# Performance work log

Measured on AMD Instinct MI355X. Metric: run time of the kernel, lower is better.

## Reference

```python
import jax, jax.numpy as jnp
import numpy as np

B, SEQ_LEN, PRED_LEN, LABEL_LEN, PERIOD, N_CH = 32, 2048, 1024, 512, 256, 256
K = SEQ_LEN // PERIOD   # seg_num_x = 8
L = PRED_LEN // PERIOD  # seg_num_y = 4
EPS = 1e-5


def setup_inputs() -> dict:
    key = jax.random.key(0)
    k1, k2, k3, k4, k5, k6, k7 = jax.random.split(key, 7)
    x_enc = jax.random.normal(k1, (B, SEQ_LEN, N_CH), jnp.float32)
    x_mark_enc = jax.random.normal(k2, (B, SEQ_LEN, 4), jnp.float32)
    x_dec = jax.random.normal(k3, (B, LABEL_LEN + PRED_LEN, N_CH), jnp.float32)
    x_mark_dec = jax.random.normal(k4, (B, LABEL_LEN + PRED_LEN, 4), jnp.float32)
    # base_model abstracted as a linear map on the time axis of a [B, PERIOD, N] segment.
    # Scaled ~1/sqrt(P) so repeated powers (up to K+L-1 = 11) stay numerically tame.
    W_base = jax.random.normal(k5, (PERIOD, PERIOD), jnp.float32) * (0.9 / np.sqrt(PERIOD))
    # new_encoders[j]: nn.Linear(seg_num_x, 1) -> weight row [K] + bias scalar per j.
    W_enc = jax.random.normal(k6, (L, K), jnp.float32) * (1.0 / np.sqrt(K))
    b_enc = jax.random.normal(k7, (L,), jnp.float32) * 0.01
    return {"x_enc": x_enc, "x_mark_enc": x_mark_enc, "x_dec": x_dec,
            "x_mark_dec": x_mark_dec, "W_base": W_base, "W_enc": W_enc, "b_enc": b_enc}


def reference(x_enc, x_mark_enc, x_dec, x_mark_dec, W_base, W_enc, b_enc):
    Bv, S, N = x_enc.shape
    # per-series normalization over time (means is .detach()'d in torch; fwd math identical)
    means = jnp.mean(x_enc, axis=1, keepdims=True)                  # [B,1,N]
    xc = x_enc - means
    stdev = jnp.sqrt(jnp.var(xc, axis=1, keepdims=True) + EPS)      # [B,1,N]
    xn = xc / stdev

    # split into K segments of length PERIOD: [K, B, P, N]
    segs = xn.reshape(Bv, K, PERIOD, N).transpose(1, 0, 2, 3)

    # x_res[l][k] = base_model applied (K - k + l) times to segment k.
    # base(x) = einsum('qp,bpn->bqn', W_base, x), so m applications = W_base^m.
    def step(c, _):
        nxt = W_base @ c
        return nxt, nxt
    _, rest = jax.lax.scan(step, W_base, None, length=K + L - 2)
    powers = jnp.concatenate([W_base[None], rest], axis=0)          # powers[i] = W^(i+1)

    exps = (K - jnp.arange(K))[None, :] + jnp.arange(L)[:, None]    # [L,K]
    Wlk = powers[exps - 1]                                          # [L,K,P,P]
    x_res = jnp.einsum('lkqp,kbpn->lkbqn', Wlk, segs)               # [L,K,B,P,N]

    # dec_out_part[l] = sum_k W_enc[l,k] * x_res[l][k] + b_enc[l] * ones
    dec = jnp.einsum('lk,lkbqn->lbqn', W_enc, x_res) + b_enc[:, None, None, None]
    dec = dec.transpose(1, 0, 2, 3).reshape(Bv, L * PERIOD, N)      # cat over time

    # de-normalize
    dec = dec * stdev[:, 0, :][:, None, :] + means[:, 0, :][:, None, :]
    return dec[:, -PRED_LEN:, :]
```

## Files before the change

kernel.cpp:

```cpp
#include <hip/hip_runtime.h>
#include <cstdint>
#include <cstddef>


typedef unsigned short ushort_t;
typedef unsigned int uint_t;
typedef __attribute__((ext_vector_type(8))) short bf16x8;
typedef __attribute__((ext_vector_type(16))) float f32x16;

__device__ __forceinline__ ushort_t f32_to_bf16(float f) {
    uint_t u = __float_as_uint(f);
    u += 0x7FFFu + ((u >> 16) & 1u);
    return (ushort_t)(u >> 16);
}
__device__ __forceinline__ float bf16_to_f32(ushort_t h) {
    return __uint_as_float((uint_t)h << 16);
}

struct PowOps { int sa[4]; int sb[4]; int sd[4]; int ed[4]; };

__global__ void powmulc(const float* __restrict__ Wb, float* __restrict__ Pw,
                        ushort_t* __restrict__ Pb, float* __restrict__ prs, PowOps ops) {
    __shared__ float As[4 * 256];
    __shared__ float red[4][4];
    const int mat = blockIdx.x;
    const int r0  = blockIdx.y * 4;
    const int tid = threadIdx.x;
    const int e   = ops.ed[mat];
    const int sa  = ops.sa[mat];
    float a[4];
    if (sa == -2) {
#pragma unroll
        for (int i = 0; i < 4; ++i) a[i] = (r0 + i == tid) ? 1.0f : 0.0f;
    } else if (sa == -3) {
#pragma unroll
        for (int i = 0; i < 4; ++i) a[i] = Wb[(size_t)(r0 + i) * 256 + tid];
    } else {
        const float* A  = (sa < 0) ? Wb : Pw + (size_t)sa * 65536;
        const float* Bm = (ops.sb[mat] < 0) ? Wb : Pw + (size_t)ops.sb[mat] * 65536;
#pragma unroll
        for (int i = 0; i < 4; ++i) As[i * 256 + tid] = A[(size_t)(r0 + i) * 256 + tid];
        __syncthreads();
        float a0 = 0.f, a1 = 0.f, a2 = 0.f, a3 = 0.f;
        for (int p = 0; p < 256; p += 8) {
            float bv[8];
#pragma unroll
            for (int u = 0; u < 8; ++u) bv[u] = Bm[(size_t)(p + u) * 256 + tid];
#pragma unroll
            for (int u = 0; u < 8; ++u) {
                a0 += As[0 * 256 + p + u] * bv[u];
                a1 += As[1 * 256 + p + u] * bv[u];
                a2 += As[2 * 256 + p + u] * bv[u];
                a3 += As[3 * 256 + p + u] * bv[u];
            }
        }
        a[0] = a0; a[1] = a1; a[2] = a2; a[3] = a3;
        if (ops.sd[mat] >= 0) {
            float* C = Pw + (size_t)ops.sd[mat] * 65536;
#pragma unroll
            for (int i = 0; i < 4; ++i) C[(size_t)(r0 + i) * 256 + tid] = a[i];
        }
        __syncthreads();
    }
    const int lane = tid & 63, wv = tid >> 6;
    float rs[4];
#pragma unroll
    for (int i = 0; i < 4; ++i) {
        const ushort_t h = f32_to_bf16(a[i]);
        Pb[(size_t)e * 65536 + (size_t)(r0 + i) * 256 + tid] = h;
        float v = bf16_to_f32(h);
        v += __shfl_xor(v, 1);  v += __shfl_xor(v, 2);  v += __shfl_xor(v, 4);
        v += __shfl_xor(v, 8);  v += __shfl_xor(v, 16); v += __shfl_xor(v, 32);
        rs[i] = v;
    }
    if (lane == 0) {
#pragma unroll
        for (int i = 0; i < 4; ++i) red[i][wv] = rs[i];
    }
    __syncthreads();
    if (tid < 4) prs[e * 256 + r0 + tid] = red[tid][0] + red[tid][1] + red[tid][2] + red[tid][3];
}

__global__ void prep(const float* __restrict__ x, ushort_t* __restrict__ Xt,
                     float* __restrict__ ps1, float* __restrict__ ps2) {
    __shared__ float lds[64 * 65];
    __shared__ float red1[16 * 64];
    __shared__ float red2[16 * 64];
    const int bid = blockIdx.x;
    const int st = bid & 31;
    const int nt = (bid >> 5) & 3;
    const int b  = bid >> 7;
    const int tid = threadIdx.x;
    const int c = tid & 15, r = tid >> 4;
    const int s0 = st * 64;
    float s1[4] = {0,0,0,0}, s2[4] = {0,0,0,0};
#pragma unroll
    for (int it = 0; it < 4; ++it) {
        const int ii = r + it * 16;
        const float4 v = *(const float4*)(x + ((size_t)b * 2048 + s0 + ii) * 256 + nt * 64 + c * 4);
        const float vv[4] = {v.x, v.y, v.z, v.w};
#pragma unroll
        for (int jj = 0; jj < 4; ++jj) {
            lds[ii * 65 + c * 4 + jj] = vv[jj];
            s1[jj] += vv[jj]; s2[jj] += vv[jj] * vv[jj];
        }
    }
#pragma unroll
    for (int jj = 0; jj < 4; ++jj) { red1[r * 64 + c * 4 + jj] = s1[jj]; red2[r * 64 + c * 4 + jj] = s2[jj]; }
    __syncthreads();
    if (tid < 64) {
        float a = 0.f, q = 0.f;
#pragma unroll
        for (int rr = 0; rr < 16; ++rr) { a += red1[rr * 64 + tid]; q += red2[rr * 64 + tid]; }
        const size_t o = (size_t)st * 8192 + b * 256 + nt * 64 + tid;
        ps1[o] = a; ps2[o] = q;
    }
#pragma unroll
    for (int step = 0; step < 8; ++step) {
        const int npr = step * 8 + (tid >> 5);
        const int sp  = (tid & 31) * 2;
        const float f0 = lds[sp * 65 + npr];
        const float f1 = lds[(sp + 1) * 65 + npr];
        const uint_t packed = (uint_t)f32_to_bf16(f0) | ((uint_t)f32_to_bf16(f1) << 16);
        *(uint_t*)(Xt + ((size_t)b * 256 + nt * 64 + npr) * 2048 + s0 + sp) = packed;
    }
}

#define GLOAD_LDS16(gsrc, ldst) \
    __builtin_amdgcn_global_load_lds((const __attribute__((address_space(1))) void*)(gsrc), \
                                     (__attribute__((address_space(3))) void*)(ldst), 16, 0, 0)

__global__ __launch_bounds__(256, 2) void gemm_v(
    const ushort_t* __restrict__ Pb,
    const ushort_t* __restrict__ Xt,
    ushort_t* __restrict__ vt)
{
    __shared__ ushort_t sAa[3][4096];
    __shared__ ushort_t sBb[3][8192];

    const int bid = blockIdx.x;
    const int tid = threadIdx.x;

    const int xcd  = bid & 7;
    const int g    = bid >> 3;
    const int colT = xcd + ((g & 7) << 3);
    const int k    = g >> 3;
    const int e    = 8 - k;

    const int lane = tid & 63;
    const int w    = tid >> 6;
    const int wm   = w >> 1, wn = w & 1;
    const int li   = lane & 31, lg = lane >> 5;
    const int lq3  = (li >> 1) & 3;
    const int lrow = 2 * (lane >> 3) + ((lane >> 2) & 1);
    const int kc   = (lane & 3) ^ ((lane >> 3) & 3);

    const ushort_t* xtb = Xt + (size_t)(colT * 128) * 2048 + k * 256;
    const ushort_t* pbb = Pb + (size_t)e * 65536;

#define VSTAGE(bf_, kt_) do { \
    const int p0_ = (kt_) * 32 + kc * 8; \
    GLOAD_LDS16(xtb + (size_t)(w * 32 + 0  + lrow) * 2048 + p0_, &sAa[bf_][(w * 32 + 0)  * 32]); \
    GLOAD_LDS16(xtb + (size_t)(w * 32 + 16 + lrow) * 2048 + p0_, &sAa[bf_][(w * 32 + 16) * 32]); \
    GLOAD_LDS16(pbb + (w * 64 + 0  + lrow) * 256 + p0_, &sBb[bf_][(w * 64 + 0)  * 32]); \
    GLOAD_LDS16(pbb + (w * 64 + 16 + lrow) * 256 + p0_, &sBb[bf_][(w * 64 + 16) * 32]); \
    GLOAD_LDS16(pbb + (w * 64 + 32 + lrow) * 256 + p0_, &sBb[bf_][(w * 64 + 32) * 32]); \
    GLOAD_LDS16(pbb + (w * 64 + 48 + lrow) * 256 + p0_, &sBb[bf_][(w * 64 + 48) * 32]); \
} while (0)

    f32x16 acc[2][4];
#pragma unroll
    for (int mm = 0; mm < 2; ++mm)
#pragma unroll
        for (int nn = 0; nn < 4; ++nn)
#pragma unroll
            for (int rr = 0; rr < 16; ++rr) acc[mm][nn][rr] = 0.0f;

    VSTAGE(0, 0);
    VSTAGE(1, 1);

#define VKT(kt_) do { \
    if ((kt_) < 7) { asm volatile("s_waitcnt vmcnt(6)" ::: "memory"); } \
    else           { asm volatile("s_waitcnt vmcnt(0)" ::: "memory"); } \
    __builtin_amdgcn_s_barrier(); \
    asm volatile("" ::: "memory"); \
    const ushort_t* pa_ = &sAa[(kt_) % 3][0]; \
    const ushort_t* px_ = &sBb[(kt_) % 3][0]; \
    bf16x8 af[2][2], xf[2][4]; \
    _Pragma("unroll") \
    for (int ks = 0; ks < 2; ++ks) { \
        const int sl = ((ks << 1) + lg) ^ lq3; \
        const int ro = (li >> 1) * 64 + (li & 1) * 32 + sl * 8; \
        af[ks][0] = *(const bf16x8*)(pa_ + wm * 2048 + ro); \
        af[ks][1] = *(const bf16x8*)(pa_ + wm * 2048 + 1024 + ro); \
        xf[ks][0] = *(const bf16x8*)(px_ + wn * 4096 + ro); \
        xf[ks][1] = *(const bf16x8*)(px_ + wn * 4096 + 1024 + ro); \
        xf[ks][2] = *(const bf16x8*)(px_ + wn * 4096 + 2048 + ro); \
        xf[ks][3] = *(const bf16x8*)(px_ + wn * 4096 + 3072 + ro); \
    } \
    if ((kt_) < 6) { VSTAGE(((kt_) + 2) % 3, (kt_) + 2); } \
    __builtin_amdgcn_s_setprio(1); \
    _Pragma("unroll") \
    for (int ks = 0; ks < 2; ++ks) \
        _Pragma("unroll") \
        for (int mm = 0; mm < 2; ++mm) \
            _Pragma("unroll") \
            for (int nn = 0; nn < 4; ++nn) \
                acc[mm][nn] = __builtin_amdgcn_mfma_f32_32x32x16_bf16(af[ks][mm], xf[ks][nn], acc[mm][nn], 0, 0, 0); \
    __builtin_amdgcn_s_setprio(0); \
    asm volatile("" ::: "memory"); \
} while (0)

    VKT(0); VKT(1); VKT(2); VKT(3); VKT(4); VKT(5); VKT(6); VKT(7);
#undef VKT
#undef VSTAGE

    ushort_t* vb = vt + (size_t)k * 2097152;
#pragma unroll
    for (int mm = 0; mm < 2; ++mm)
#pragma unroll
        for (int nn = 0; nn < 4; ++nn) {
            const int q = wn * 128 + nn * 32 + li;
#pragma unroll
            for (int rr = 0; rr < 16; ++rr) {
                const int c = colT * 128 + wm * 64 + mm * 32 + ((rr & 3) + 8 * (rr >> 2) + 4 * lg);
                vb[(size_t)c * 256 + q] = f32_to_bf16(acc[mm][nn][rr]);
            }
        }
}

__global__ void combine(const ushort_t* __restrict__ vt, const float* __restrict__ Wenc,
                        ushort_t* __restrict__ c,
                        const float* __restrict__ ps1, const float* __restrict__ ps2,
                        const float* __restrict__ prs, const ushort_t* __restrict__ Pb,
                        float* __restrict__ meanv, float* __restrict__ stdv,
                        float* __restrict__ rsA) {
    __shared__ float uf[256];
    const int bid = blockIdx.x;
    const int t   = threadIdx.x;
    if (bid < 1024) {
        const int col = bid * 8 + (t >> 5);
        const size_t off = (size_t)col * 256 + (t & 31) * 8;
        float a0[8] = {0,0,0,0,0,0,0,0}, a1[8] = {0,0,0,0,0,0,0,0};
        float a2[8] = {0,0,0,0,0,0,0,0}, a3[8] = {0,0,0,0,0,0,0,0};
#pragma unroll
        for (int k = 0; k < 8; ++k) {
            const bf16x8 v = *(const bf16x8*)(vt + (size_t)k * 2097152 + off);
            const float w0 = Wenc[0 * 8 + k], w1 = Wenc[1 * 8 + k];
            const float w2 = Wenc[2 * 8 + k], w3 = Wenc[3 * 8 + k];
#pragma unroll
            for (int j = 0; j < 8; ++j) {
                const float f = bf16_to_f32((ushort_t)v[j]);
                a0[j] += w0 * f; a1[j] += w1 * f; a2[j] += w2 * f; a3[j] += w3 * f;
            }
        }
        bf16x8 o0, o1, o2, o3;
#pragma unroll
        for (int j = 0; j < 8; ++j) {
            o0[j] = (short)f32_to_bf16(a0[j]); o1[j] = (short)f32_to_bf16(a1[j]);
            o2[j] = (short)f32_to_bf16(a2[j]); o3[j] = (short)f32_to_bf16(a3[j]);
        }
        *(bf16x8*)(c + 0 * 2097152 + off) = o0;
        *(bf16x8*)(c + 1 * 2097152 + off) = o1;
        *(bf16x8*)(c + 2 * 2097152 + off) = o2;
        *(bf16x8*)(c + 3 * 2097152 + off) = o3;
    } else if (bid < 1056) {
        const int b = bid - 1024;
        float s = 0.f, q = 0.f;
#pragma unroll
        for (int st = 0; st < 32; ++st) {
            s += ps1[(size_t)st * 8192 + b * 256 + t];
            q += ps2[(size_t)st * 8192 + b * 256 + t];
        }
        const float mean = s * (1.0f / 2048.0f);
        float var = q * (1.0f / 2048.0f) - mean * mean;
        var = fmaxf(var, 0.0f);
        meanv[b * 256 + t] = mean;
        stdv [b * 256 + t] = sqrtf(var + 1e-5f);
    } else {
        const int l = bid - 1056;
        float u = 0.f;
#pragma unroll
        for (int k = 0; k < 8; ++k) u += Wenc[l * 8 + k] * prs[(8 - k) * 256 + t];
        uf[t] = u;
        __syncthreads();
        const uint2* rp = (const uint2*)(Pb + (size_t)l * 65536 + t * 256);
        float s = 0.f;
#pragma unroll
        for (int i = 0; i < 64; ++i) {
            const uint2 v = rp[i];
            s += bf16_to_f32((ushort_t)(v.x & 0xffff)) * uf[i * 4 + 0]
               + bf16_to_f32((ushort_t)(v.x >> 16))    * uf[i * 4 + 1]
               + bf16_to_f32((ushort_t)(v.y & 0xffff)) * uf[i * 4 + 2]
               + bf16_to_f32((ushort_t)(v.y >> 16))    * uf[i * 4 + 3];
        }
        rsA[l * 256 + t] = s;
    }
}

__global__ __launch_bounds__(256, 2) void gemm2(
    const ushort_t* __restrict__ Pb, const ushort_t* __restrict__ c,
    const float* __restrict__ meanv, const float* __restrict__ stdv,
    const float* __restrict__ rsA, const float* __restrict__ benc,
    float* __restrict__ out)
{
    __shared__ ushort_t sAa[3][4096];
    __shared__ ushort_t sBb[3][4096];

    const int bid  = blockIdx.x;
    const int xcd  = bid & 7;
    const int g    = bid >> 3;
    const int colT = xcd + ((g & 7) << 3);
    const int rest = g >> 3;
    const int l    = rest >> 1;
    const int qpT  = rest & 1;

    const int tid  = threadIdx.x;
    const int lane = tid & 63;
    const int w    = tid >> 6;
    const int wm   = w >> 1, wn = w & 1;
    const int li   = lane & 31, lg = lane >> 5;
    const int lq3  = (li >> 1) & 3;
    const int lrow = 2 * (lane >> 3) + ((lane >> 2) & 1);
    const int kc   = (lane & 3) ^ ((lane >> 3) & 3);

    const ushort_t* ab = Pb + (size_t)l * 65536 + (size_t)(qpT * 128) * 256;
    const ushort_t* cb = c + ((size_t)l * 8192 + colT * 128) * 256;

#define GSTAGE(bf_, kt_) do { \
    const int p0_ = (kt_) * 32 + kc * 8; \
    GLOAD_LDS16(ab + (w * 32 + 0  + lrow) * 256 + p0_, &sAa[bf_][(w * 32 + 0)  * 32]); \
    GLOAD_LDS16(ab + (w * 32 + 16 + lrow) * 256 + p0_, &sAa[bf_][(w * 32 + 16) * 32]); \
    GLOAD_LDS16(cb + (w * 32 + 0  + lrow) * 256 + p0_, &sBb[bf_][(w * 32 + 0)  * 32]); \
    GLOAD_LDS16(cb + (w * 32 + 16 + lrow) * 256 + p0_, &sBb[bf_][(w * 32 + 16) * 32]); \
} while (0)

    f32x16 acc[2][2];
#pragma unroll
    for (int mm = 0; mm < 2; ++mm)
#pragma unroll
        for (int nn = 0; nn < 2; ++nn)
#pragma unroll
            for (int rr = 0; rr < 16; ++rr) acc[mm][nn][rr] = 0.0f;

    GSTAGE(0, 0);
    GSTAGE(1, 1);

#define GKT(kt_) do { \
    if ((kt_) < 7) { asm volatile("s_waitcnt vmcnt(4)" ::: "memory"); } \
    else           { asm volatile("s_waitcnt vmcnt(0)" ::: "memory"); } \
    __builtin_amdgcn_s_barrier(); \
    asm volatile("" ::: "memory"); \
    const ushort_t* pa_ = &sAa[(kt_) % 3][0]; \
    const ushort_t* px_ = &sBb[(kt_) % 3][0]; \
    bf16x8 af[2][2], xf[2][2]; \
    _Pragma("unroll") \
    for (int ks = 0; ks < 2; ++ks) { \
        const int sl = ((ks << 1) + lg) ^ lq3; \
        const int ro = (li >> 1) * 64 + (li & 1) * 32 + sl * 8; \
        af[ks][0] = *(const bf16x8*)(pa_ + wm * 2048 + ro); \
        af[ks][1] = *(const bf16x8*)(pa_ + wm * 2048 + 1024 + ro); \
        xf[ks][0] = *(const bf16x8*)(px_ + wn * 2048 + ro); \
        xf[ks][1] = *(const bf16x8*)(px_ + wn * 2048 + 1024 + ro); \
    } \
    if ((kt_) < 6) { GSTAGE(((kt_) + 2) % 3, (kt_) + 2); } \
    __builtin_amdgcn_s_setprio(1); \
    _Pragma("unroll") \
    for (int ks = 0; ks < 2; ++ks) { \
        acc[0][0] = __builtin_amdgcn_mfma_f32_32x32x16_bf16(af[ks][0], xf[ks][0], acc[0][0], 0, 0, 0); \
        acc[0][1] = __builtin_amdgcn_mfma_f32_32x32x16_bf16(af[ks][0], xf[ks][1], acc[0][1], 0, 0, 0); \
        acc[1][0] = __builtin_amdgcn_mfma_f32_32x32x16_bf16(af[ks][1], xf[ks][0], acc[1][0], 0, 0, 0); \
        acc[1][1] = __builtin_amdgcn_mfma_f32_32x32x16_bf16(af[ks][1], xf[ks][1], acc[1][1], 0, 0, 0); \
    } \
    __builtin_amdgcn_s_setprio(0); \
    asm volatile("" ::: "memory"); \
} while (0)

    GKT(0); GKT(1); GKT(2); GKT(3); GKT(4); GKT(5); GKT(6); GKT(7);
#undef GKT
#undef GSTAGE

    const float be = benc[l];
    float mn[2], sd[2];
#pragma unroll
    for (int nn = 0; nn < 2; ++nn) {
        const int col = colT * 128 + wn * 64 + nn * 32 + li;
        mn[nn] = meanv[col];
        sd[nn] = stdv [col];
    }
#pragma unroll
    for (int mm = 0; mm < 2; ++mm)
#pragma unroll
        for (int nn = 0; nn < 2; ++nn) {
            const int col = colT * 128 + wn * 64 + nn * 32 + li;
            const int bq = col >> 8, nq = col & 255;
            const float ben = be * sd[nn];
#pragma unroll
            for (int rr = 0; rr < 16; ++rr) {
                const int trow = l * 256 + qpT * 128 + wm * 64 + mm * 32
                               + ((rr & 3) + 8 * (rr >> 2) + 4 * lg);
                out[((size_t)bq * 1024 + trow) * 256 + nq] =
                    acc[mm][nn][rr] + mn[nn] * (1.0f - rsA[trow]) + ben;
            }
        }
}

extern "C" void kernel_launch(void* const* d_in, const int* in_sizes, int n_in,
                              void* d_out, int out_size, void* d_ws, size_t ws_size,
                              hipStream_t stream) {
    (void)in_sizes; (void)n_in; (void)out_size; (void)ws_size;
    const float* x_enc  = (const float*)d_in[0];
    const float* W_base = (const float*)d_in[4];
    const float* W_enc  = (const float*)d_in[5];
    const float* b_enc  = (const float*)d_in[6];
    float* out = (float*)d_out;

    char* ws = (char*)d_ws;
    float*    wsP    = (float*)(ws);
    ushort_t* wsPb   = (ushort_t*)(ws + 0x200000);
    float*    wsPrs  = (float*)(ws + 0x340000);
    float*    wsS1   = (float*)(ws + 0x350000);
    float*    wsS2   = (float*)(ws + 0x450000);
    float*    wsMean = (float*)(ws + 0x550000);
    float*    wsStd  = (float*)(ws + 0x560000);
    float*    wsRsA  = (float*)(ws + 0x570000);
    ushort_t* wsXt   = (ushort_t*)(ws + 0x600000);
    ushort_t* wsC    = (ushort_t*)(ws + 0x600000);
    ushort_t* wsVt   = (ushort_t*)(ws + 0x2600000);

    { PowOps o{{-1, -3, -2, 0}, {-1, 0, 0, 0}, {0, -1, -1, 0}, {2, 1, 0, 0}};
      powmulc<<<dim3(3, 64), 256, 0, stream>>>(W_base, wsP, wsPb, wsPrs, o); }
    { PowOps o{{0, 0, 0, 0}, {-1, 0, 0, 0}, {1, 2, 0, 0}, {3, 4, 0, 0}};
      powmulc<<<dim3(2, 64), 256, 0, stream>>>(W_base, wsP, wsPb, wsPrs, o); }
    { PowOps o{{2, 2, 2, 2}, {-1, 0, 1, 2}, {-1, -1, -1, -1}, {5, 6, 7, 8}};
      powmulc<<<dim3(4, 64), 256, 0, stream>>>(W_base, wsP, wsPb, wsPrs, o); }

    prep<<<4096, 256, 0, stream>>>(x_enc, wsXt, wsS1, wsS2);

    gemm_v<<<512, 256, 0, stream>>>(wsPb, wsXt, wsVt);

    combine<<<1060, 256, 0, stream>>>(wsVt, W_enc, wsC, wsS1, wsS2, wsPrs, wsPb,
                                      wsMean, wsStd, wsRsA);

    gemm2<<<512, 256, 0, stream>>>(wsPb, wsC, wsMean, wsStd, wsRsA, b_enc, out);
}
```

Before: 99.64 us.

## Fuse combine into second GEMM and fold stats/rowsum into gemm_v

Removes the separate combine kernel. The W_enc-weighted reduction over the eight vt slices now runs inside a new 512-thread gemm2c kernel, which writes the combined bf16 tile straight to LDS and feeds it to MFMA, so the intermediate c buffer never goes through global memory. The mean/std and rsA side computations move into extra blocks appended to the gemm_v launch. This saves one launch and a full write-plus-read of c, but each gemm2c block reads all eight vt slices per k-tile, and it changes the block count, LDS footprint and occupancy.

```diff
diff --git a/kernel.cpp b/kernel.cpp
--- a/kernel.cpp
+++ b/kernel.cpp
@@ -133,13 +133,53 @@
 __global__ __launch_bounds__(256, 2) void gemm_v(
     const ushort_t* __restrict__ Pb,
     const ushort_t* __restrict__ Xt,
-    ushort_t* __restrict__ vt)
+    ushort_t* __restrict__ vt,
+    const float* __restrict__ ps1, const float* __restrict__ ps2,
+    const float* __restrict__ prs, const float* __restrict__ Wenc,
+    float* __restrict__ meanv, float* __restrict__ stdv, float* __restrict__ rsA)
 {
     __shared__ ushort_t sAa[3][4096];
     __shared__ ushort_t sBb[3][8192];
 
     const int bid = blockIdx.x;
     const int tid = threadIdx.x;
+    if (bid >= 512) {
+        const int idx = bid - 512;
+        if (idx < 32) {
+            const int b = idx;
+            float s = 0.f, q = 0.f;
+#pragma unroll
+            for (int st = 0; st < 32; ++st) {
+                s += ps1[(size_t)st * 8192 + b * 256 + tid];
+                q += ps2[(size_t)st * 8192 + b * 256 + tid];
+            }
+            const float mean = s * (1.0f / 2048.0f);
+            float var = q * (1.0f / 2048.0f) - mean * mean;
+            var = fmaxf(var, 0.0f);
+            meanv[b * 256 + tid] = mean;
+            stdv [b * 256 + tid] = sqrtf(var + 1e-5f);
+        } else {
+            const int l = idx - 32;
+            float u = 0.f;
+#pragma unroll
+            for (int k = 0; k < 8; ++k) u += Wenc[l * 8 + k] * prs[(8 - k) * 256 + tid];
+            float* uf = (float*)&sAa[0][0];
+            uf[tid] = u;
+            __syncthreads();
+            const uint2* rp = (const uint2*)(Pb + (size_t)l * 65536 + tid * 256);
+            float s = 0.f;
+#pragma unroll
+            for (int i = 0; i < 64; ++i) {
+                const uint2 v = rp[i];
+                s += bf16_to_f32((ushort_t)(v.x & 0xffff)) * uf[i * 4 + 0]
+                   + bf16_to_f32((ushort_t)(v.x >> 16))    * uf[i * 4 + 1]
+                   + bf16_to_f32((ushort_t)(v.y & 0xffff)) * uf[i * 4 + 2]
+                   + bf16_to_f32((ushort_t)(v.y >> 16))    * uf[i * 4 + 3];
+            }
+            rsA[l * 256 + tid] = s;
+        }
+        return;
+    }
 
     const int xcd  = bid & 7;
     const int g    = bid >> 3;
@@ -229,110 +269,80 @@
         }
 }
 
-__global__ void combine(const ushort_t* __restrict__ vt, const float* __restrict__ Wenc,
-                        ushort_t* __restrict__ c,
-                        const float* __restrict__ ps1, const float* __restrict__ ps2,
-                        const float* __restrict__ prs, const ushort_t* __restrict__ Pb,
-                        float* __restrict__ meanv, float* __restrict__ stdv,
-                        float* __restrict__ rsA) {
-    __shared__ float uf[256];
-    const int bid = blockIdx.x;
-    const int t   = threadIdx.x;
-    if (bid < 1024) {
-        const int col = bid * 8 + (t >> 5);
-        const size_t off = (size_t)col * 256 + (t & 31) * 8;
-        float a0[8] = {0,0,0,0,0,0,0,0}, a1[8] = {0,0,0,0,0,0,0,0};
-        float a2[8] = {0,0,0,0,0,0,0,0}, a3[8] = {0,0,0,0,0,0,0,0};
-#pragma unroll
-        for (int k = 0; k < 8; ++k) {
-            const bf16x8 v = *(const bf16x8*)(vt + (size_t)k * 2097152 + off);
-            const float w0 = Wenc[0 * 8 + k], w1 = Wenc[1 * 8 + k];
-            const float w2 = Wenc[2 * 8 + k], w3 = Wenc[3 * 8 + k];
-#pragma unroll
-            for (int j = 0; j < 8; ++j) {
-                const float f = bf16_to_f32((ushort_t)v[j]);
-                a0[j] += w0 * f; a1[j] += w1 * f; a2[j] += w2 * f; a3[j] += w3 * f;
-            }
-        }
-        bf16x8 o0, o1, o2, o3;
-#pragma unroll
-        for (int j = 0; j < 8; ++j) {
-            o0[j] = (short)f32_to_bf16(a0[j]); o1[j] = (short)f32_to_bf16(a1[j]);
-            o2[j] = (short)f32_to_bf16(a2[j]); o3[j] = (short)f32_to_bf16(a3[j]);
-        }
-        *(bf16x8*)(c + 0 * 2097152 + off) = o0;
-        *(bf16x8*)(c + 1 * 2097152 + off) = o1;
-        *(bf16x8*)(c + 2 * 2097152 + off) = o2;
-        *(bf16x8*)(c + 3 * 2097152 + off) = o3;
-    } else if (bid < 1056) {
-        const int b = bid - 1024;
-        float s = 0.f, q = 0.f;
-#pragma unroll
-        for (int st = 0; st < 32; ++st) {
-            s += ps1[(size_t)st * 8192 + b * 256 + t];
-            q += ps2[(size_t)st * 8192 + b * 256 + t];
-        }
-        const float mean = s * (1.0f / 2048.0f);
-        float var = q * (1.0f / 2048.0f) - mean * mean;
-        var = fmaxf(var, 0.0f);
-        meanv[b * 256 + t] = mean;
-        stdv [b * 256 + t] = sqrtf(var + 1e-5f);
-    } else {
-        const int l = bid - 1056;
-        float u = 0.f;
-#pragma unroll
-        for (int k = 0; k < 8; ++k) u += Wenc[l * 8 + k] * prs[(8 - k) * 256 + t];
-        uf[t] = u;
-        __syncthreads();
-        const uint2* rp = (const uint2*)(Pb + (size_t)l * 65536 + t * 256);
-        float s = 0.f;
-#pragma unroll
-        for (int i = 0; i < 64; ++i) {
-            const uint2 v = rp[i];
-            s += bf16_to_f32((ushort_t)(v.x & 0xffff)) * uf[i * 4 + 0]
-               + bf16_to_f32((ushort_t)(v.x >> 16))    * uf[i * 4 + 1]
-               + bf16_to_f32((ushort_t)(v.y & 0xffff)) * uf[i * 4 + 2]
-               + bf16_to_f32((ushort_t)(v.y >> 16))    * uf[i * 4 + 3];
-        }
-        rsA[l * 256 + t] = s;
-    }
-}
-
-__global__ __launch_bounds__(256, 2) void gemm2(
-    const ushort_t* __restrict__ Pb, const ushort_t* __restrict__ c,
+__global__ __launch_bounds__(512, 2) void gemm2c(
+    const ushort_t* __restrict__ Pb, const ushort_t* __restrict__ vt,
+    const float* __restrict__ Wenc,
     const float* __restrict__ meanv, const float* __restrict__ stdv,
     const float* __restrict__ rsA, const float* __restrict__ benc,
     float* __restrict__ out)
 {
-    __shared__ ushort_t sAa[3][4096];
-    __shared__ ushort_t sBb[3][4096];
+    __shared__ ushort_t sAa[3][16384];
+    __shared__ ushort_t sCc[2][8192];
 
     const int bid  = blockIdx.x;
     const int xcd  = bid & 7;
     const int g    = bid >> 3;
-    const int colT = xcd + ((g & 7) << 3);
-    const int rest = g >> 3;
-    const int l    = rest >> 1;
-    const int qpT  = rest & 1;
+    const int colH = xcd + ((g & 15) << 3);
+    const int qc   = g >> 4;
 
     const int tid  = threadIdx.x;
     const int lane = tid & 63;
     const int w    = tid >> 6;
-    const int wm   = w >> 1, wn = w & 1;
+    const int l    = w & 3;
+    const int qh   = w >> 2;
     const int li   = lane & 31, lg = lane >> 5;
     const int lq3  = (li >> 1) & 3;
     const int lrow = 2 * (lane >> 3) + ((lane >> 2) & 1);
     const int kc   = (lane & 3) ^ ((lane >> 3) & 3);
 
-    const ushort_t* ab = Pb + (size_t)l * 65536 + (size_t)(qpT * 128) * 256;
-    const ushort_t* cb = c + ((size_t)l * 8192 + colT * 128) * 256;
-
-#define GSTAGE(bf_, kt_) do { \
+    const int ccol = tid & 63;
+    const int qoct = (tid >> 6) & 3;
+    const int rep  = tid >> 8;
+
+    const ushort_t* ab = Pb + (size_t)l * 65536 + (size_t)(qc * 128) * 256;
+    const ushort_t* vb = vt + (size_t)(colH * 64 + ccol) * 256;
+
+    float weR[2][8];
+#pragma unroll
+    for (int j = 0; j < 2; ++j)
+#pragma unroll
+        for (int k = 0; k < 8; ++k) weR[j][k] = Wenc[(rep * 2 + j) * 8 + k];
+    asm volatile("s_waitcnt vmcnt(0)" ::: "memory");
+
+#define AST(bf_, kt_) do { \
     const int p0_ = (kt_) * 32 + kc * 8; \
-    GLOAD_LDS16(ab + (w * 32 + 0  + lrow) * 256 + p0_, &sAa[bf_][(w * 32 + 0)  * 32]); \
-    GLOAD_LDS16(ab + (w * 32 + 16 + lrow) * 256 + p0_, &sAa[bf_][(w * 32 + 16) * 32]); \
-    GLOAD_LDS16(cb + (w * 32 + 0  + lrow) * 256 + p0_, &sBb[bf_][(w * 32 + 0)  * 32]); \
-    GLOAD_LDS16(cb + (w * 32 + 16 + lrow) * 256 + p0_, &sBb[bf_][(w * 32 + 16) * 32]); \
+    _Pragma("unroll") \
+    for (int i_ = 0; i_ < 4; ++i_) \
+        GLOAD_LDS16(ab + (size_t)(qh * 64 + i_ * 16 + lrow) * 256 + p0_, \
+                    &sAa[bf_][l * 4096 + qh * 2048 + i_ * 512]); \
+} while (0)
+
+#define VLOAD(dst_, kt_) do { \
+    _Pragma("unroll") \
+    for (int k_ = 0; k_ < 8; ++k_) \
+        dst_[k_] = *(const bf16x8*)(vb + (size_t)k_ * 2097152 + (kt_) * 32 + qoct * 8); \
+} while (0)
+
+#define COMB(src_, cb_) do { \
+    _Pragma("unroll") \
+    for (int j_ = 0; j_ < 2; ++j_) { \
+        float s_[8] = {0,0,0,0,0,0,0,0}; \
+        _Pragma("unroll") \
+        for (int k_ = 0; k_ < 8; ++k_) { \
+            const float w_ = weR[j_][k_]; \
+            _Pragma("unroll") \
+            for (int q_ = 0; q_ < 8; ++q_) \
+                s_[q_] += w_ * bf16_to_f32((ushort_t)src_[k_][q_]); \
+        } \
+        uint4 o_; \
+        o_.x = (uint_t)f32_to_bf16(s_[0]) | ((uint_t)f32_to_bf16(s_[1]) << 16); \
+        o_.y = (uint_t)f32_to_bf16(s_[2]) | ((uint_t)f32_to_bf16(s_[3]) << 16); \
+        o_.z = (uint_t)f32_to_bf16(s_[4]) | ((uint_t)f32_to_bf16(s_[5]) << 16); \
+        o_.w = (uint_t)f32_to_bf16(s_[6]) | ((uint_t)f32_to_bf16(s_[7]) << 16); \
+        const int le_ = (rep * 2 + j_) * 2048 + (ccol >> 1) * 64 + (ccol & 1) * 32 \
+                      + ((qoct ^ ((ccol >> 1) & 3)) * 8); \
+        *(uint4*)(&sCc[cb_][le_]) = o_; \
+    } \
 } while (0)
 
     f32x16 acc[2][2];
@@ -343,48 +353,54 @@
 #pragma unroll
             for (int rr = 0; rr < 16; ++rr) acc[mm][nn][rr] = 0.0f;
 
-    GSTAGE(0, 0);
-    GSTAGE(1, 1);
-
-#define GKT(kt_) do { \
-    if ((kt_) < 7) { asm volatile("s_waitcnt vmcnt(4)" ::: "memory"); } \
-    else           { asm volatile("s_waitcnt vmcnt(0)" ::: "memory"); } \
+    bf16x8 vvA[8], vvB[8];
+    AST(0, 0);
+    VLOAD(vvA, 0);
+
+#define G2KT(kt_, cur_, nxt_) do { \
+    if ((kt_) < 7) { \
+        AST(((kt_) + 1) % 3, (kt_) + 1); \
+        VLOAD(nxt_, (kt_) + 1); \
+        asm volatile("s_waitcnt vmcnt(12)" ::: "memory"); \
+    } else { \
+        asm volatile("s_waitcnt vmcnt(0)" ::: "memory"); \
+    } \
+    COMB(cur_, (kt_) & 1); \
+    asm volatile("s_waitcnt lgkmcnt(0)" ::: "memory"); \
     __builtin_amdgcn_s_barrier(); \
     asm volatile("" ::: "memory"); \
-    const ushort_t* pa_ = &sAa[(kt_) % 3][0]; \
-    const ushort_t* px_ = &sBb[(kt_) % 3][0]; \
-    bf16x8 af[2][2], xf[2][2]; \
-    _Pragma("unroll") \
-    for (int ks = 0; ks < 2; ++ks) { \
-        const int sl = ((ks << 1) + lg) ^ lq3; \
-        const int ro = (li >> 1) * 64 + (li & 1) * 32 + sl * 8; \
-        af[ks][0] = *(const bf16x8*)(pa_ + wm * 2048 + ro); \
-        af[ks][1] = *(const bf16x8*)(pa_ + wm * 2048 + 1024 + ro); \
-        xf[ks][0] = *(const bf16x8*)(px_ + wn * 2048 + ro); \
-        xf[ks][1] = *(const bf16x8*)(px_ + wn * 2048 + 1024 + ro); \
-    } \
-    if ((kt_) < 6) { GSTAGE(((kt_) + 2) % 3, (kt_) + 2); } \
+    const ushort_t* pa_ = &sAa[(kt_) % 3][l * 4096 + qh * 2048]; \
+    const ushort_t* px_ = &sCc[(kt_) & 1][l * 2048]; \
     __builtin_amdgcn_s_setprio(1); \
     _Pragma("unroll") \
-    for (int ks = 0; ks < 2; ++ks) { \
-        acc[0][0] = __builtin_amdgcn_mfma_f32_32x32x16_bf16(af[ks][0], xf[ks][0], acc[0][0], 0, 0, 0); \
-        acc[0][1] = __builtin_amdgcn_mfma_f32_32x32x16_bf16(af[ks][0], xf[ks][1], acc[0][1], 0, 0, 0); \
-        acc[1][0] = __builtin_amdgcn_mfma_f32_32x32x16_bf16(af[ks][1], xf[ks][0], acc[1][0], 0, 0, 0); \
-        acc[1][1] = __builtin_amdgcn_mfma_f32_32x32x16_bf16(af[ks][1], xf[ks][1], acc[1][1], 0, 0, 0); \
+    for (int ks_ = 0; ks_ < 2; ++ks_) { \
+        const int sl_ = (ks_ * 2 + lg) ^ lq3; \
+        const int ro_ = (li >> 1) * 64 + (li & 1) * 32 + sl_ * 8; \
+        const bf16x8 a0_ = *(const bf16x8*)(pa_ + ro_); \
+        const bf16x8 a1_ = *(const bf16x8*)(pa_ + 1024 + ro_); \
+        const bf16x8 x0_ = *(const bf16x8*)(px_ + ro_); \
+        const bf16x8 x1_ = *(const bf16x8*)(px_ + 1024 + ro_); \
+        acc[0][0] = __builtin_amdgcn_mfma_f32_32x32x16_bf16(a0_, x0_, acc[0][0], 0, 0, 0); \
+        acc[0][1] = __builtin_amdgcn_mfma_f32_32x32x16_bf16(a0_, x1_, acc[0][1], 0, 0, 0); \
+        acc[1][0] = __builtin_amdgcn_mfma_f32_32x32x16_bf16(a1_, x0_, acc[1][0], 0, 0, 0); \
+        acc[1][1] = __builtin_amdgcn_mfma_f32_32x32x16_bf16(a1_, x1_, acc[1][1], 0, 0, 0); \
     } \
     __builtin_amdgcn_s_setprio(0); \
     asm volatile("" ::: "memory"); \
 } while (0)
 
-    GKT(0); GKT(1); GKT(2); GKT(3); GKT(4); GKT(5); GKT(6); GKT(7);
-#undef GKT
-#undef GSTAGE
+    G2KT(0, vvA, vvB); G2KT(1, vvB, vvA); G2KT(2, vvA, vvB); G2KT(3, vvB, vvA);
+    G2KT(4, vvA, vvB); G2KT(5, vvB, vvA); G2KT(6, vvA, vvB); G2KT(7, vvB, vvA);
+#undef G2KT
+#undef COMB
+#undef VLOAD
+#undef AST
 
     const float be = benc[l];
     float mn[2], sd[2];
 #pragma unroll
     for (int nn = 0; nn < 2; ++nn) {
-        const int col = colT * 128 + wn * 64 + nn * 32 + li;
+        const int col = colH * 64 + nn * 32 + li;
         mn[nn] = meanv[col];
         sd[nn] = stdv [col];
     }
@@ -392,12 +408,12 @@
     for (int mm = 0; mm < 2; ++mm)
 #pragma unroll
         for (int nn = 0; nn < 2; ++nn) {
-            const int col = colT * 128 + wn * 64 + nn * 32 + li;
+            const int col = colH * 64 + nn * 32 + li;
             const int bq = col >> 8, nq = col & 255;
             const float ben = be * sd[nn];
 #pragma unroll
             for (int rr = 0; rr < 16; ++rr) {
-                const int trow = l * 256 + qpT * 128 + wm * 64 + mm * 32
+                const int trow = l * 256 + qc * 128 + qh * 64 + mm * 32
                                + ((rr & 3) + 8 * (rr >> 2) + 4 * lg);
                 out[((size_t)bq * 1024 + trow) * 256 + nq] =
                     acc[mm][nn][rr] + mn[nn] * (1.0f - rsA[trow]) + ben;
@@ -425,7 +441,6 @@
     float*    wsStd  = (float*)(ws + 0x560000);
     float*    wsRsA  = (float*)(ws + 0x570000);
     ushort_t* wsXt   = (ushort_t*)(ws + 0x600000);
-    ushort_t* wsC    = (ushort_t*)(ws + 0x600000);
     ushort_t* wsVt   = (ushort_t*)(ws + 0x2600000);
 
     { PowOps o{{-1, -3, -2, 0}, {-1, 0, 0, 0}, {0, -1, -1, 0}, {2, 1, 0, 0}};
@@ -437,10 +452,9 @@
 
     prep<<<4096, 256, 0, stream>>>(x_enc, wsXt, wsS1, wsS2);
 
-    gemm_v<<<512, 256, 0, stream>>>(wsPb, wsXt, wsVt);
-
-    combine<<<1060, 256, 0, stream>>>(wsVt, W_enc, wsC, wsS1, wsS2, wsPrs, wsPb,
-                                      wsMean, wsStd, wsRsA);
-
-    gemm2<<<512, 256, 0, stream>>>(wsPb, wsC, wsMean, wsStd, wsRsA, b_enc, out);
-}
+    gemm_v<<<548, 256, 0, stream>>>(wsPb, wsXt, wsVt, wsS1, wsS2, wsPrs, W_enc,
+                                    wsMean, wsStd, wsRsA);
+
+    gemm2c<<<256, 512, 0, stream>>>(wsPb, wsVt, W_enc, wsMean, wsStd, wsRsA,
+                                    b_enc, out);
+}
```

After: 122.1 us. 1.23x slower.

## Fuse matrix-power computation into prep kernel via independent per-row repeated multiplication

Applied to the files above, without the earlier changes.

Drops the three dependent powmulc launches that built W^e by squaring and chaining, and instead has 576 extra blocks in the prep kernel each compute four rows of W^e by multiplying a row strip by W_base e-1 times. This removes two kernel launches and the serial dependency between power stages, and lets the power computation overlap with the normalization/transpose work. The cost is more total FLOPs (up to 7 sequential row-strip multiplies for the highest power), a long tail on the e=8 blocks, and slightly different rounding from the changed multiplication order.

```diff
diff --git a/kernel.cpp b/kernel.cpp
--- a/kernel.cpp
+++ b/kernel.cpp
@@ -17,80 +17,78 @@
     return __uint_as_float((uint_t)h << 16);
 }
 
-struct PowOps { int sa[4]; int sb[4]; int sd[4]; int ed[4]; };
-
-__global__ void powmulc(const float* __restrict__ Wb, float* __restrict__ Pw,
-                        ushort_t* __restrict__ Pb, float* __restrict__ prs, PowOps ops) {
-    __shared__ float As[4 * 256];
-    __shared__ float red[4][4];
-    const int mat = blockIdx.x;
-    const int r0  = blockIdx.y * 4;
+__global__ void prep_pow(const float* __restrict__ x, ushort_t* __restrict__ Xt,
+                         float* __restrict__ ps1, float* __restrict__ ps2,
+                         const float* __restrict__ Wb,
+                         ushort_t* __restrict__ Pb, float* __restrict__ prs) {
+    __shared__ float shmem[64 * 65 + 2048];
+    const int bid = blockIdx.x;
     const int tid = threadIdx.x;
-    const int e   = ops.ed[mat];
-    const int sa  = ops.sa[mat];
-    float a[4];
-    if (sa == -2) {
-#pragma unroll
-        for (int i = 0; i < 4; ++i) a[i] = (r0 + i == tid) ? 1.0f : 0.0f;
-    } else if (sa == -3) {
-#pragma unroll
-        for (int i = 0; i < 4; ++i) a[i] = Wb[(size_t)(r0 + i) * 256 + tid];
-    } else {
-        const float* A  = (sa < 0) ? Wb : Pw + (size_t)sa * 65536;
-        const float* Bm = (ops.sb[mat] < 0) ? Wb : Pw + (size_t)ops.sb[mat] * 65536;
-#pragma unroll
-        for (int i = 0; i < 4; ++i) As[i * 256 + tid] = A[(size_t)(r0 + i) * 256 + tid];
+
+    if (bid < 576) {
+        const int e  = bid >> 6;
+        const int r0 = (bid & 63) * 4;
+        float a[4];
+        if (e == 0) {
+#pragma unroll
+            for (int i = 0; i < 4; ++i) a[i] = (r0 + i == tid) ? 1.0f : 0.0f;
+        } else {
+#pragma unroll
+            for (int i = 0; i < 4; ++i) a[i] = Wb[(size_t)(r0 + i) * 256 + tid];
+            if (e >= 2) {
+                float* R = shmem;
+                for (int step = 0; step < e - 1; ++step) {
+                    __syncthreads();
+#pragma unroll
+                    for (int i = 0; i < 4; ++i) R[i * 256 + tid] = a[i];
+                    __syncthreads();
+                    float n0 = 0.f, n1 = 0.f, n2 = 0.f, n3 = 0.f;
+                    for (int p = 0; p < 256; p += 8) {
+                        float bv[8];
+#pragma unroll
+                        for (int u = 0; u < 8; ++u) bv[u] = Wb[(size_t)(p + u) * 256 + tid];
+#pragma unroll
+                        for (int u = 0; u < 8; ++u) {
+                            n0 += R[0 * 256 + p + u] * bv[u];
+                            n1 += R[1 * 256 + p + u] * bv[u];
+                            n2 += R[2 * 256 + p + u] * bv[u];
+                            n3 += R[3 * 256 + p + u] * bv[u];
+                        }
+                    }
+                    a[0] = n0; a[1] = n1; a[2] = n2; a[3] = n3;
+                }
+            }
+        }
+        const int lane = tid & 63, wv = tid >> 6;
+        float rs[4];
+#pragma unroll
+        for (int i = 0; i < 4; ++i) {
+            const ushort_t h = f32_to_bf16(a[i]);
+            Pb[(size_t)e * 65536 + (size_t)(r0 + i) * 256 + tid] = h;
+            float v = bf16_to_f32(h);
+            v += __shfl_xor(v, 1);  v += __shfl_xor(v, 2);  v += __shfl_xor(v, 4);
+            v += __shfl_xor(v, 8);  v += __shfl_xor(v, 16); v += __shfl_xor(v, 32);
+            rs[i] = v;
+        }
         __syncthreads();
-        float a0 = 0.f, a1 = 0.f, a2 = 0.f, a3 = 0.f;
-        for (int p = 0; p < 256; p += 8) {
-            float bv[8];
-#pragma unroll
-            for (int u = 0; u < 8; ++u) bv[u] = Bm[(size_t)(p + u) * 256 + tid];
-#pragma unroll
-            for (int u = 0; u < 8; ++u) {
-                a0 += As[0 * 256 + p + u] * bv[u];
-                a1 += As[1 * 256 + p + u] * bv[u];
-                a2 += As[2 * 256 + p + u] * bv[u];
-                a3 += As[3 * 256 + p + u] * bv[u];
-            }
-        }
-        a[0] = a0; a[1] = a1; a[2] = a2; a[3] = a3;
-        if (ops.sd[mat] >= 0) {
-            float* C = Pw + (size_t)ops.sd[mat] * 65536;
-#pragma unroll
-            for (int i = 0; i < 4; ++i) C[(size_t)(r0 + i) * 256 + tid] = a[i];
+        float* red = shmem;
+        if (lane == 0) {
+#pragma unroll
+            for (int i = 0; i < 4; ++i) red[i * 4 + wv] = rs[i];
         }
         __syncthreads();
-    }
-    const int lane = tid & 63, wv = tid >> 6;
-    float rs[4];
-#pragma unroll
-    for (int i = 0; i < 4; ++i) {
-        const ushort_t h = f32_to_bf16(a[i]);
-        Pb[(size_t)e * 65536 + (size_t)(r0 + i) * 256 + tid] = h;
-        float v = bf16_to_f32(h);
-        v += __shfl_xor(v, 1);  v += __shfl_xor(v, 2);  v += __shfl_xor(v, 4);
-        v += __shfl_xor(v, 8);  v += __shfl_xor(v, 16); v += __shfl_xor(v, 32);
-        rs[i] = v;
-    }
-    if (lane == 0) {
-#pragma unroll
-        for (int i = 0; i < 4; ++i) red[i][wv] = rs[i];
-    }
-    __syncthreads();
-    if (tid < 4) prs[e * 256 + r0 + tid] = red[tid][0] + red[tid][1] + red[tid][2] + red[tid][3];
-}
-
-__global__ void prep(const float* __restrict__ x, ushort_t* __restrict__ Xt,
-                     float* __restrict__ ps1, float* __restrict__ ps2) {
-    __shared__ float lds[64 * 65];
-    __shared__ float red1[16 * 64];
-    __shared__ float red2[16 * 64];
-    const int bid = blockIdx.x;
-    const int st = bid & 31;
-    const int nt = (bid >> 5) & 3;
-    const int b  = bid >> 7;
-    const int tid = threadIdx.x;
+        if (tid < 4) prs[e * 256 + r0 + tid] = red[tid * 4 + 0] + red[tid * 4 + 1]
+                                             + red[tid * 4 + 2] + red[tid * 4 + 3];
+        return;
+    }
+
+    const int pb = bid - 576;
+    const int st = pb & 31;
+    const int nt = (pb >> 5) & 3;
+    const int b  = pb >> 7;
+    float* lds  = shmem;
+    float* red1 = shmem + 64 * 65;
+    float* red2 = red1 + 1024;
     const int c = tid & 15, r = tid >> 4;
     const int s0 = st * 64;
     float s1[4] = {0,0,0,0}, s2[4] = {0,0,0,0};
@@ -416,7 +414,6 @@
     float* out = (float*)d_out;
 
     char* ws = (char*)d_ws;
-    float*    wsP    = (float*)(ws);
     ushort_t* wsPb   = (ushort_t*)(ws + 0x200000);
     float*    wsPrs  = (float*)(ws + 0x340000);
     float*    wsS1   = (float*)(ws + 0x350000);
@@ -428,14 +425,7 @@
     ushort_t* wsC    = (ushort_t*)(ws + 0x600000);
     ushort_t* wsVt   = (ushort_t*)(ws + 0x2600000);
 
-    { PowOps o{{-1, -3, -2, 0}, {-1, 0, 0, 0}, {0, -1, -1, 0}, {2, 1, 0, 0}};
-      powmulc<<<dim3(3, 64), 256, 0, stream>>>(W_base, wsP, wsPb, wsPrs, o); }
-    { PowOps o{{0, 0, 0, 0}, {-1, 0, 0, 0}, {1, 2, 0, 0}, {3, 4, 0, 0}};
-      powmulc<<<dim3(2, 64), 256, 0, stream>>>(W_base, wsP, wsPb, wsPrs, o); }
-    { PowOps o{{2, 2, 2, 2}, {-1, 0, 1, 2}, {-1, -1, -1, -1}, {5, 6, 7, 8}};
-      powmulc<<<dim3(4, 64), 256, 0, stream>>>(W_base, wsP, wsPb, wsPrs, o); }
-
-    prep<<<4096, 256, 0, stream>>>(x_enc, wsXt, wsS1, wsS2);
+    prep_pow<<<4672, 256, 0, stream>>>(x_enc, wsXt, wsS1, wsS2, W_base, wsPb, wsPrs);
 
     gemm_v<<<512, 256, 0, stream>>>(wsPb, wsXt, wsVt);
 
```

Result: slower. 104.0 us (+4.4%).
